# Performance work log

Hardware: AMD Instinct MI355X
Metric: run time of the kernel (lower is better)

## Reference

```python
import jax, jax.numpy as jnp
import numpy as np

TEMPERATURE = 0.07
N_BANK = 1_000_000
DIM = 128
BATCH = 1024
K_NEIGH = 200


def _prob_density(memory_bank, v, idx):
    # memory_bank: [N, D], v: [B, D] (L2-normalized), idx: [B, K]
    vals = memory_bank[idx]                      # [B, K, D] gather
    dots = jnp.einsum('bkd,bd->bk', vals, v)     # per-item dot products
    return jnp.sum(jnp.exp(dots / TEMPERATURE), axis=1)  # [B]


def setup_inputs() -> dict:
    key = jax.random.key(0)
    k1, k2, k3, k4 = jax.random.split(key, 4)
    codes = jax.random.normal(k1, (BATCH, DIM), dtype=jnp.float32)
    memory_bank = jax.random.normal(k2, (N_BANK, DIM), dtype=jnp.float32)
    # memory bank rows are unit-normalized in the LA setup
    memory_bank = memory_bank / jnp.linalg.norm(memory_bank, axis=1, keepdims=True)
    idx_background = jax.random.randint(k3, (BATCH, K_NEIGH), 0, N_BANK, dtype=jnp.int64)
    idx_close = jax.random.randint(k4, (BATCH, K_NEIGH), 0, N_BANK, dtype=jnp.int64)
    return {
        'codes': codes,
        'memory_bank': memory_bank,
        'idx_background': idx_background,
        'idx_close': idx_close,
    }


def reference(codes, memory_bank, idx_background, idx_close):
    # v = F.normalize(codes, p=2, dim=1)
    v = codes / jnp.linalg.norm(codes, axis=1, keepdims=True)
    d1 = _prob_density(memory_bank, v, idx_background)
    d2 = _prob_density(memory_bank, v, idx_close)
    # loss_cluster = log(d1) - log(d2)
    return jnp.log(d1) - jnp.log(d2)
```

## Files before the change

kernel.cpp:

```cpp
#include <hip/hip_runtime.h>
#include <math.h>


constexpr int DIM   = 128;
constexpr int KN    = 200;
constexpr float INV_T = 1.0f / 0.07f;

__global__ __launch_bounds__(256, 4)
void lal_kernel(const float* __restrict__ codes,
                const float* __restrict__ bank,
                const int*   __restrict__ idx_bg,
                const int*   __restrict__ idx_cl,
                float*       __restrict__ out)
{
    const int b   = blockIdx.x;
    const int tid = threadIdx.x;

    __shared__ float v[DIM];
    __shared__ float wsum[4];
    __shared__ float red1[8];
    __shared__ float red2[8];
    __shared__ float s_rnorm;

    float c  = (tid < DIM) ? codes[b * DIM + tid] : 0.0f;
    float ss = c * c;
    #pragma unroll
    for (int m = 32; m > 0; m >>= 1) ss += __shfl_xor(ss, m, 64);
    if ((tid & 63) == 0) wsum[tid >> 6] = ss;
    __syncthreads();
    if (tid == 0) {
        float t = wsum[0] + wsum[1] + wsum[2] + wsum[3];
        s_rnorm = 1.0f / sqrtf(t);
    }
    __syncthreads();
    if (tid < DIM) v[tid] = c * s_rnorm;
    __syncthreads();

    const int group = tid >> 5;
    const int lane  = tid & 31;

    const float4 vv = ((const float4*)v)[lane];

    const int* ib = idx_bg + b * KN;
    const int* ic = idx_cl + b * KN;

    float sum1 = 0.0f, sum2 = 0.0f;
    for (int k = group; k < KN; k += 8) {
        const int r1 = ib[k];
        const int r2 = ic[k];
        const float4 x1 = ((const float4*)(bank + (size_t)r1 * DIM))[lane];
        const float4 x2 = ((const float4*)(bank + (size_t)r2 * DIM))[lane];
        float d1 = x1.x * vv.x + x1.y * vv.y + x1.z * vv.z + x1.w * vv.w;
        float d2 = x2.x * vv.x + x2.y * vv.y + x2.z * vv.z + x2.w * vv.w;
        #pragma unroll
        for (int m = 16; m > 0; m >>= 1) {
            d1 += __shfl_xor(d1, m, 64);
            d2 += __shfl_xor(d2, m, 64);
        }
        sum1 += expf(d1 * INV_T);
        sum2 += expf(d2 * INV_T);
    }

    if (lane == 0) { red1[group] = sum1; red2[group] = sum2; }
    __syncthreads();
    if (tid == 0) {
        float D1 = 0.0f, D2 = 0.0f;
        #pragma unroll
        for (int g = 0; g < 8; ++g) { D1 += red1[g]; D2 += red2[g]; }
        out[b] = logf(D1) - logf(D2);
    }
}

extern "C" void kernel_launch(void* const* d_in, const int* in_sizes, int n_in,
                              void* d_out, int out_size, void* d_ws, size_t ws_size,
                              hipStream_t stream)
{
    const float* codes  = (const float*)d_in[0];
    const float* bank   = (const float*)d_in[1];
    const int*   idx_bg = (const int*)d_in[2];
    const int*   idx_cl = (const int*)d_in[3];
    float*       out    = (float*)d_out;

    const int batch = in_sizes[0] / DIM;
    lal_kernel<<<batch, 256, 0, stream>>>(codes, bank, idx_bg, idx_cl, out);
}
```

Measured before the change: 591.1 us.

## Split gather across chunked blocks with register-batched loads and atomic accumulation

Splits the work into three kernels: one normalizes codes into workspace, one gathers bank rows with each batch row split across five blocks, and one takes the final logs. Each warp-half prefetches its five indices and issues all row loads up front, with the close-set loads overlapping the background dot products. The goal is more memory-level parallelism and more blocks in flight for this latency-bound random gather. The cost is two extra launches, float atomics (summation order becomes nondeterministic), and fast __expf in place of expf.

```diff
diff --git a/kernel.cpp b/kernel.cpp
--- a/kernel.cpp
+++ b/kernel.cpp
@@ -2,73 +2,94 @@
 #include <math.h>
 
 
-constexpr int DIM   = 128;
-constexpr int KN    = 200;
+constexpr int DIM    = 128;
+constexpr int KN     = 200;
+constexpr int CHUNKS = 5;
+constexpr int RPC    = KN / CHUNKS;
+constexpr int RPG    = RPC / 8;
 constexpr float INV_T = 1.0f / 0.07f;
 
-__global__ __launch_bounds__(256, 4)
-void lal_kernel(const float* __restrict__ codes,
-                const float* __restrict__ bank,
-                const int*   __restrict__ idx_bg,
-                const int*   __restrict__ idx_cl,
-                float*       __restrict__ out)
+__global__ __launch_bounds__(64)
+void prep_kernel(const float* __restrict__ codes,
+                 float* __restrict__ ws_v,
+                 float* __restrict__ acc)
 {
-    const int b   = blockIdx.x;
-    const int tid = threadIdx.x;
-
-    __shared__ float v[DIM];
-    __shared__ float wsum[4];
-    __shared__ float red1[8];
-    __shared__ float red2[8];
-    __shared__ float s_rnorm;
-
-    float c  = (tid < DIM) ? codes[b * DIM + tid] : 0.0f;
-    float ss = c * c;
+    const int b = blockIdx.x;
+    const int t = threadIdx.x;
+    float2 c2 = ((const float2*)(codes + (size_t)b * DIM))[t];
+    float ss = c2.x * c2.x + c2.y * c2.y;
     #pragma unroll
     for (int m = 32; m > 0; m >>= 1) ss += __shfl_xor(ss, m, 64);
-    if ((tid & 63) == 0) wsum[tid >> 6] = ss;
-    __syncthreads();
-    if (tid == 0) {
-        float t = wsum[0] + wsum[1] + wsum[2] + wsum[3];
-        s_rnorm = 1.0f / sqrtf(t);
-    }
-    __syncthreads();
-    if (tid < DIM) v[tid] = c * s_rnorm;
-    __syncthreads();
+    const float rn = 1.0f / sqrtf(ss);
+    float2 o; o.x = c2.x * rn; o.y = c2.y * rn;
+    ((float2*)(ws_v + (size_t)b * DIM))[t] = o;
+    if (t < 2) acc[b * 2 + t] = 0.0f;
+}
 
-    const int group = tid >> 5;
+__global__ __launch_bounds__(256, 8)
+void gather_kernel(const float* __restrict__ bank,
+                   const float* __restrict__ ws_v,
+                   const int*   __restrict__ idx_bg,
+                   const int*   __restrict__ idx_cl,
+                   float*       __restrict__ acc)
+{
+    const int b     = blockIdx.x;
+    const int chunk = blockIdx.y;
+    const int tid   = threadIdx.x;
+    const int g     = tid >> 5;
     const int lane  = tid & 31;
 
-    const float4 vv = ((const float4*)v)[lane];
+    const float4 vv = ((const float4*)(ws_v + (size_t)b * DIM))[lane];
 
-    const int* ib = idx_bg + b * KN;
-    const int* ic = idx_cl + b * KN;
+    const int kb = chunk * RPC + g * RPG;
+    const int* ib = idx_bg + b * KN + kb;
+    const int* ic = idx_cl + b * KN + kb;
+
+    int r1[RPG], r2[RPG];
+    #pragma unroll
+    for (int u = 0; u < RPG; ++u) { r1[u] = ib[u]; r2[u] = ic[u]; }
 
     float sum1 = 0.0f, sum2 = 0.0f;
-    for (int k = group; k < KN; k += 8) {
-        const int r1 = ib[k];
-        const int r2 = ic[k];
-        const float4 x1 = ((const float4*)(bank + (size_t)r1 * DIM))[lane];
-        const float4 x2 = ((const float4*)(bank + (size_t)r2 * DIM))[lane];
-        float d1 = x1.x * vv.x + x1.y * vv.y + x1.z * vv.z + x1.w * vv.w;
-        float d2 = x2.x * vv.x + x2.y * vv.y + x2.z * vv.z + x2.w * vv.w;
+    float4 x[RPG];
+
+    #pragma unroll
+    for (int u = 0; u < RPG; ++u)
+        x[u] = ((const float4*)(bank + (size_t)r1[u] * DIM))[lane];
+
+    #pragma unroll
+    for (int u = 0; u < RPG; ++u) {
+        const float4 xu = x[u];
+        x[u] = ((const float4*)(bank + (size_t)r2[u] * DIM))[lane];
+        float d = xu.x * vv.x + xu.y * vv.y + xu.z * vv.z + xu.w * vv.w;
         #pragma unroll
-        for (int m = 16; m > 0; m >>= 1) {
-            d1 += __shfl_xor(d1, m, 64);
-            d2 += __shfl_xor(d2, m, 64);
-        }
-        sum1 += expf(d1 * INV_T);
-        sum2 += expf(d2 * INV_T);
+        for (int m = 16; m > 0; m >>= 1) d += __shfl_xor(d, m, 64);
+        sum1 += __expf(d * INV_T);
+    }
+    #pragma unroll
+    for (int u = 0; u < RPG; ++u) {
+        float d = x[u].x * vv.x + x[u].y * vv.y + x[u].z * vv.z + x[u].w * vv.w;
+        #pragma unroll
+        for (int m = 16; m > 0; m >>= 1) d += __shfl_xor(d, m, 64);
+        sum2 += __expf(d * INV_T);
     }
 
-    if (lane == 0) { red1[group] = sum1; red2[group] = sum2; }
+    __shared__ float red1[8], red2[8];
+    if (lane == 0) { red1[g] = sum1; red2[g] = sum2; }
     __syncthreads();
     if (tid == 0) {
         float D1 = 0.0f, D2 = 0.0f;
         #pragma unroll
-        for (int g = 0; g < 8; ++g) { D1 += red1[g]; D2 += red2[g]; }
-        out[b] = logf(D1) - logf(D2);
+        for (int i = 0; i < 8; ++i) { D1 += red1[i]; D2 += red2[i]; }
+        atomicAdd(&acc[b * 2 + 0], D1);
+        atomicAdd(&acc[b * 2 + 1], D2);
     }
+}
+
+__global__ void finish_kernel(const float* __restrict__ acc,
+                              float* __restrict__ out, int batch)
+{
+    const int i = blockIdx.x * blockDim.x + threadIdx.x;
+    if (i < batch) out[i] = logf(acc[2 * i]) - logf(acc[2 * i + 1]);
 }
 
 extern "C" void kernel_launch(void* const* d_in, const int* in_sizes, int n_in,
@@ -82,5 +103,11 @@
     float*       out    = (float*)d_out;
 
     const int batch = in_sizes[0] / DIM;
-    lal_kernel<<<batch, 256, 0, stream>>>(codes, bank, idx_bg, idx_cl, out);
+
+    float* ws_v = (float*)d_ws;
+    float* acc  = ws_v + (size_t)batch * DIM;
+
+    prep_kernel<<<batch, 64, 0, stream>>>(codes, ws_v, acc);
+    gather_kernel<<<dim3(batch, CHUNKS), 256, 0, stream>>>(bank, ws_v, idx_bg, idx_cl, acc);
+    finish_kernel<<<(batch + 255) / 256, 256, 0, stream>>>(acc, out, batch);
 }
```

Measured after the change: 590.3 us. Within noise of the previous version (-0.1%).
